# Performance work log

Measured on AMD Instinct MI355X. Metric: run time of the kernel, lower is better.

The kernel has to match this reference:

```python
import jax, jax.numpy as jnp
import numpy as np

N_NODES = 100000
N_EDGES = 1600000
F_IN = 128
UNITS = 128


def setup_inputs() -> dict:
    key = jax.random.key(0)
    k1, k2, k3, k4, k5 = jax.random.split(key, 5)
    X = jax.random.normal(k1, (N_NODES, F_IN), dtype=jnp.float32)
    edge_row = jnp.sort(jax.random.randint(k2, (N_EDGES,), 0, N_NODES, dtype=jnp.int64))
    edge_col = jax.random.randint(k3, (N_EDGES,), 0, N_NODES, dtype=jnp.int64)
    edge_val = jax.random.uniform(k4, (N_EDGES,), dtype=jnp.float32)
    weight = jax.random.normal(k5, (F_IN, UNITS), dtype=jnp.float32) * (1.0 / np.sqrt(F_IN))
    bias = jnp.zeros((UNITS,), dtype=jnp.float32)
    return {"X": X, "edge_row": edge_row, "edge_col": edge_col,
            "edge_val": edge_val, "weight": weight, "bias": bias}


def reference(X, edge_row, edge_col, edge_val, weight, bias):
    # h = X @ W  (dense feature transform)
    h = jnp.matmul(X, weight)                      # [N, units]
    # output = An @ h  as sparse SpMM: gather source rows, scale, scatter-add
    msg = edge_val[:, None] * h[edge_col]          # [E, units]
    agg = jax.ops.segment_sum(msg, edge_row, num_segments=N_NODES)  # [N, units]
    # bias add + sigmoid activation
    return jax.nn.sigmoid(agg + bias)
```

## Files before the change

### kernel.cpp

```cpp
#include <hip/hip_runtime.h>
#include <cstddef>

#define F 128
#define LDB 136

typedef __attribute__((ext_vector_type(8))) short bf16x8;
typedef __attribute__((ext_vector_type(4))) float f32x4;

__device__ __forceinline__ unsigned short f2bf(float f) {
  unsigned int u = __float_as_uint(f);
  u += 0x7fffu + ((u >> 16) & 1u);
  return (unsigned short)(u >> 16);
}

__global__ __launch_bounds__(256) void setup(const int* __restrict__ erow,
                                             int n_edges, int n_nodes, int nbA,
                                             int* __restrict__ row_ptr,
                                             const float* __restrict__ W,
                                             unsigned short* __restrict__ Wt) {
  const int bid = blockIdx.x;
  if (bid < nbA) {
    const int e = bid * 256 + threadIdx.x;
    if (e > n_edges) return;
    int r_lo, r_hi, val;
    if (e == 0) {
      r_lo = 0; r_hi = erow[0]; val = 0;
    } else if (e == n_edges) {
      r_lo = erow[n_edges - 1] + 1; r_hi = n_nodes; val = n_edges;
    } else {
      const int rp = erow[e - 1], rc = erow[e];
      r_lo = rp + 1; r_hi = rc; val = e;
    }
    for (int r = r_lo; r <= r_hi; ++r) row_ptr[r] = val;
  } else {
    const int idx = (bid - nbA) * 256 + threadIdx.x;
    const int k = idx >> 7, n = idx & 127;
    Wt[n * F + k] = f2bf(W[idx]);
  }
}

__global__ __launch_bounds__(256) void gemm_mfma(const float* __restrict__ X,
                                                 const unsigned short* __restrict__ Wt,
                                                 unsigned short* __restrict__ H,
                                                 int n_nodes) {
  __shared__ alignas(16) unsigned short Bs[128 * LDB];
  const int tid = threadIdx.x;

  {
    const uint4* src = (const uint4*)Wt;
    #pragma unroll
    for (int i = 0; i < 8; ++i) {
      const int idx = tid + i * 256;
      const int n = idx >> 4, c8 = idx & 15;
      *(uint4*)&Bs[n * LDB + c8 * 8] = src[idx];
    }
  }
  __syncthreads();

  const int wave = tid >> 6;
  const int lane = tid & 63;
  const int l15 = lane & 15;
  const int quad = lane >> 4;
  const int rbase = blockIdx.x * 128 + wave * 32;

  const float* xr[2];
  #pragma unroll
  for (int rt = 0; rt < 2; ++rt) {
    int r = rbase + rt * 16 + l15;
    if (r > n_nodes - 1) r = n_nodes - 1;
    xr[rt] = X + (size_t)r * F;
  }

  f32x4 acc[2][8] = {};

  #pragma unroll
  for (int ks = 0; ks < 4; ++ks) {
    const int k0 = ks * 32 + quad * 8;
    bf16x8 a[2], b[8];
    #pragma unroll
    for (int rt = 0; rt < 2; ++rt) {
      const float4 x0 = *(const float4*)(xr[rt] + k0);
      const float4 x1 = *(const float4*)(xr[rt] + k0 + 4);
      bf16x8 t;
      t[0] = (short)f2bf(x0.x); t[1] = (short)f2bf(x0.y);
      t[2] = (short)f2bf(x0.z); t[3] = (short)f2bf(x0.w);
      t[4] = (short)f2bf(x1.x); t[5] = (short)f2bf(x1.y);
      t[6] = (short)f2bf(x1.z); t[7] = (short)f2bf(x1.w);
      a[rt] = t;
    }
    #pragma unroll
    for (int ct = 0; ct < 8; ++ct)
      b[ct] = *(const bf16x8*)&Bs[(ct * 16 + l15) * LDB + k0];
    #pragma unroll
    for (int rt = 0; rt < 2; ++rt)
      #pragma unroll
      for (int ct = 0; ct < 8; ++ct)
        acc[rt][ct] = __builtin_amdgcn_mfma_f32_16x16x32_bf16(
            b[ct], a[rt], acc[rt][ct], 0, 0, 0);
  }

  #pragma unroll
  for (int rt = 0; rt < 2; ++rt) {
    const int row = rbase + rt * 16 + l15;
    if (row < n_nodes) {
      #pragma unroll
      for (int ct = 0; ct < 8; ++ct) {
        const unsigned int d0 = (unsigned int)f2bf(acc[rt][ct][0]) |
                                ((unsigned int)f2bf(acc[rt][ct][1]) << 16);
        const unsigned int d1 = (unsigned int)f2bf(acc[rt][ct][2]) |
                                ((unsigned int)f2bf(acc[rt][ct][3]) << 16);
        uint2 u; u.x = d0; u.y = d1;
        *(uint2*)&H[(size_t)row * F + ct * 16 + quad * 4] = u;
      }
    }
  }
}

__global__ __launch_bounds__(256) void spmm_bias_sigmoid(
    const int* __restrict__ row_ptr, const int* __restrict__ ecol,
    const float* __restrict__ eval, const unsigned short* __restrict__ H,
    const float* __restrict__ bias, float* __restrict__ out, int n_nodes) {
  const int wave = threadIdx.x >> 6;
  const int lane = threadIdx.x & 63;
  const int g = lane >> 4;
  const int fl = lane & 15;
  const int node = blockIdx.x * 16 + wave * 4 + g;
  const bool valid = (node < n_nodes);

  const int lo = valid ? row_ptr[node] : 0;
  const int hi = valid ? row_ptr[node + 1] : 0;
  const int deg = hi - lo;

  int dmax = deg;
  dmax = max(dmax, __shfl_xor(dmax, 16, 64));
  dmax = max(dmax, __shfl_xor(dmax, 32, 64));

  const int bpbase = (lane & 48) * 4;
  const char* Hb = (const char*)H + fl * 16;

  float acc[8] = {};

#define SPMM_STEP(j)                                                        \
  {                                                                         \
    const int idx = bpbase + (j) * 4;                                       \
    const int ro = __builtin_amdgcn_ds_bpermute(idx, voff);                 \
    const float v = __int_as_float(                                         \
        __builtin_amdgcn_ds_bpermute(idx, __float_as_int(vv)));             \
    const uint4 h = *(const uint4*)(Hb + ro);                               \
    acc[0] += v * __uint_as_float(h.x << 16);                               \
    acc[1] += v * __uint_as_float(h.x & 0xffff0000u);                       \
    acc[2] += v * __uint_as_float(h.y << 16);                               \
    acc[3] += v * __uint_as_float(h.y & 0xffff0000u);                       \
    acc[4] += v * __uint_as_float(h.z << 16);                               \
    acc[5] += v * __uint_as_float(h.z & 0xffff0000u);                       \
    acc[6] += v * __uint_as_float(h.w << 16);                               \
    acc[7] += v * __uint_as_float(h.w & 0xffff0000u);                       \
  }

  for (int base = 0; base < dmax; base += 16) {
    int voff = 0;
    float vv = 0.f;
    if (base + fl < deg) {
      const int e = lo + base + fl;
      voff = ecol[e] << 8;
      vv = eval[e];
    }
    const int cnt = min(dmax - base, 16);
    if (cnt == 16) {
      #pragma unroll
      for (int j = 0; j < 16; ++j) SPMM_STEP(j)
    } else {
      #pragma unroll 4
      for (int j = 0; j < cnt; ++j) SPMM_STEP(j)
    }
  }
#undef SPMM_STEP

  if (valid) {
    const float4 b0 = *(const float4*)&bias[fl * 8];
    const float4 b1 = *(const float4*)&bias[fl * 8 + 4];
    float4 o0, o1;
    o0.x = 1.f / (1.f + expf(-(acc[0] + b0.x)));
    o0.y = 1.f / (1.f + expf(-(acc[1] + b0.y)));
    o0.z = 1.f / (1.f + expf(-(acc[2] + b0.z)));
    o0.w = 1.f / (1.f + expf(-(acc[3] + b0.w)));
    o1.x = 1.f / (1.f + expf(-(acc[4] + b1.x)));
    o1.y = 1.f / (1.f + expf(-(acc[5] + b1.y)));
    o1.z = 1.f / (1.f + expf(-(acc[6] + b1.z)));
    o1.w = 1.f / (1.f + expf(-(acc[7] + b1.w)));
    float* op = out + (size_t)node * F + fl * 8;
    *(float4*)op = o0;
    *(float4*)(op + 4) = o1;
  }
}

extern "C" void kernel_launch(void* const* d_in, const int* in_sizes, int n_in,
                              void* d_out, int out_size, void* d_ws, size_t ws_size,
                              hipStream_t stream) {
  const float* X    = (const float*)d_in[0];
  const int*   erow = (const int*)  d_in[1];
  const int*   ecol = (const int*)  d_in[2];
  const float* eval = (const float*)d_in[3];
  const float* W    = (const float*)d_in[4];
  const float* bias = (const float*)d_in[5];
  float* out = (float*)d_out;

  const int n_nodes = in_sizes[0] / F;
  const int n_edges = in_sizes[1];

  char* ws = (char*)d_ws;
  unsigned short* H = (unsigned short*)ws;
  size_t off = (size_t)n_nodes * F * sizeof(unsigned short);
  int* row_ptr = (int*)(ws + off);
  off += ((size_t)(n_nodes + 1) * sizeof(int) + 15) & ~(size_t)15;
  unsigned short* Wt = (unsigned short*)(ws + off);

  const int nbA = (n_edges + 256) / 256;
  const int nbB = (F * F) / 256;
  setup<<<nbA + nbB, 256, 0, stream>>>(erow, n_edges, n_nodes, nbA, row_ptr,
                                       W, Wt);
  gemm_mfma<<<(n_nodes + 127) / 128, 256, 0, stream>>>(X, Wt, H, n_nodes);
  spmm_bias_sigmoid<<<(n_nodes + 15) / 16, 256, 0, stream>>>(
      row_ptr, ecol, eval, H, bias, out, n_nodes);
}
```

Baseline: 189.7 us.

## Slice H into 16-feature column panels and process SpMM per feature slice

The GEMM now writes H as eight column-major panels of 16 bf16 features each (32 bytes per node per panel). The SpMM kernel is split across 8 feature-slice blocks per 128-node tile. Each pair of lanes owns one node and walks its edges with 4-wide nontemporal loads of col/val, replacing the earlier 16-lane cooperative gather with ds_bpermute broadcasts. The intent is for each panel (about 3.2 MB) to fit in cache so gathers hit L2, at the cost of reading edge lists eight times and uneven per-lane degree work within a wave.

```diff
diff --git a/kernel.cpp b/kernel.cpp
--- a/kernel.cpp
+++ b/kernel.cpp
@@ -6,6 +6,7 @@
 
 typedef __attribute__((ext_vector_type(8))) short bf16x8;
 typedef __attribute__((ext_vector_type(4))) float f32x4;
+typedef __attribute__((ext_vector_type(4))) unsigned int u32x4;
 
 __device__ __forceinline__ unsigned short f2bf(float f) {
   unsigned int u = __float_as_uint(f);
@@ -99,6 +100,7 @@
             b[ct], a[rt], acc[rt][ct], 0, 0, 0);
   }
 
+  const size_t ns16 = (size_t)n_nodes * 16;
   #pragma unroll
   for (int rt = 0; rt < 2; ++rt) {
     const int row = rbase + rt * 16 + l15;
@@ -110,87 +112,74 @@
         const unsigned int d1 = (unsigned int)f2bf(acc[rt][ct][2]) |
                                 ((unsigned int)f2bf(acc[rt][ct][3]) << 16);
         uint2 u; u.x = d0; u.y = d1;
-        *(uint2*)&H[(size_t)row * F + ct * 16 + quad * 4] = u;
+        *(uint2*)&H[ns16 * ct + (size_t)row * 16 + quad * 4] = u;
       }
     }
   }
+}
+
+__device__ __forceinline__ void fma8(float* acc, uint4 h, float v) {
+  acc[0] += v * __uint_as_float(h.x << 16);
+  acc[1] += v * __uint_as_float(h.x & 0xffff0000u);
+  acc[2] += v * __uint_as_float(h.y << 16);
+  acc[3] += v * __uint_as_float(h.y & 0xffff0000u);
+  acc[4] += v * __uint_as_float(h.z << 16);
+  acc[5] += v * __uint_as_float(h.z & 0xffff0000u);
+  acc[6] += v * __uint_as_float(h.w << 16);
+  acc[7] += v * __uint_as_float(h.w & 0xffff0000u);
 }
 
 __global__ __launch_bounds__(256) void spmm_bias_sigmoid(
     const int* __restrict__ row_ptr, const int* __restrict__ ecol,
     const float* __restrict__ eval, const unsigned short* __restrict__ H,
     const float* __restrict__ bias, float* __restrict__ out, int n_nodes) {
+  const int fb = blockIdx.x & 7;
+  const int nb = blockIdx.x >> 3;
+  const int lane = threadIdx.x & 63;
   const int wave = threadIdx.x >> 6;
-  const int lane = threadIdx.x & 63;
-  const int g = lane >> 4;
-  const int fl = lane & 15;
-  const int node = blockIdx.x * 16 + wave * 4 + g;
+  const int p = lane & 1;
+  const int node = nb * 128 + wave * 32 + (lane >> 1);
   const bool valid = (node < n_nodes);
 
-  const int lo = valid ? row_ptr[node] : 0;
-  const int hi = valid ? row_ptr[node + 1] : 0;
-  const int deg = hi - lo;
-
-  int dmax = deg;
-  dmax = max(dmax, __shfl_xor(dmax, 16, 64));
-  dmax = max(dmax, __shfl_xor(dmax, 32, 64));
-
-  const int bpbase = (lane & 48) * 4;
-  const char* Hb = (const char*)H + fl * 16;
+  int lo = 0, deg = 0;
+  if (valid) {
+    lo = row_ptr[node];
+    deg = row_ptr[node + 1] - lo;
+  }
+
+  const char* Hs = (const char*)H + (size_t)fb * ((size_t)n_nodes * 32) +
+                   (size_t)(p * 16);
 
   float acc[8] = {};
 
-#define SPMM_STEP(j)                                                        \
-  {                                                                         \
-    const int idx = bpbase + (j) * 4;                                       \
-    const int ro = __builtin_amdgcn_ds_bpermute(idx, voff);                 \
-    const float v = __int_as_float(                                         \
-        __builtin_amdgcn_ds_bpermute(idx, __float_as_int(vv)));             \
-    const uint4 h = *(const uint4*)(Hb + ro);                               \
-    acc[0] += v * __uint_as_float(h.x << 16);                               \
-    acc[1] += v * __uint_as_float(h.x & 0xffff0000u);                       \
-    acc[2] += v * __uint_as_float(h.y << 16);                               \
-    acc[3] += v * __uint_as_float(h.y & 0xffff0000u);                       \
-    acc[4] += v * __uint_as_float(h.z << 16);                               \
-    acc[5] += v * __uint_as_float(h.z & 0xffff0000u);                       \
-    acc[6] += v * __uint_as_float(h.w << 16);                               \
-    acc[7] += v * __uint_as_float(h.w & 0xffff0000u);                       \
-  }
-
-  for (int base = 0; base < dmax; base += 16) {
-    int voff = 0;
-    float vv = 0.f;
-    if (base + fl < deg) {
-      const int e = lo + base + fl;
-      voff = ecol[e] << 8;
-      vv = eval[e];
-    }
-    const int cnt = min(dmax - base, 16);
-    if (cnt == 16) {
-      #pragma unroll
-      for (int j = 0; j < 16; ++j) SPMM_STEP(j)
-    } else {
-      #pragma unroll 4
-      for (int j = 0; j < cnt; ++j) SPMM_STEP(j)
-    }
-  }
-#undef SPMM_STEP
+  const int abase = lo & ~3;
+  const int aend = (lo + deg + 3) & ~3;
+  for (int e0 = abase; e0 < aend; e0 += 4) {
+    const u32x4 cols = __builtin_nontemporal_load((const u32x4*)(ecol + e0));
+    const f32x4 vals = __builtin_nontemporal_load((const f32x4*)(eval + e0));
+    #pragma unroll
+    for (int j = 0; j < 4; ++j) {
+      const unsigned rel = (unsigned)(e0 + j - lo);
+      const float v = (rel < (unsigned)deg) ? vals[j] : 0.f;
+      const uint4 h = *(const uint4*)(Hs + ((size_t)cols[j] << 5));
+      fma8(acc, h, v);
+    }
+  }
 
   if (valid) {
-    const float4 b0 = *(const float4*)&bias[fl * 8];
-    const float4 b1 = *(const float4*)&bias[fl * 8 + 4];
-    float4 o0, o1;
-    o0.x = 1.f / (1.f + expf(-(acc[0] + b0.x)));
-    o0.y = 1.f / (1.f + expf(-(acc[1] + b0.y)));
-    o0.z = 1.f / (1.f + expf(-(acc[2] + b0.z)));
-    o0.w = 1.f / (1.f + expf(-(acc[3] + b0.w)));
-    o1.x = 1.f / (1.f + expf(-(acc[4] + b1.x)));
-    o1.y = 1.f / (1.f + expf(-(acc[5] + b1.y)));
-    o1.z = 1.f / (1.f + expf(-(acc[6] + b1.z)));
-    o1.w = 1.f / (1.f + expf(-(acc[7] + b1.w)));
-    float* op = out + (size_t)node * F + fl * 8;
-    *(float4*)op = o0;
-    *(float4*)(op + 4) = o1;
+    const float* bp = bias + fb * 16 + p * 8;
+    f32x4 o0, o1;
+    o0[0] = 1.f / (1.f + expf(-(acc[0] + bp[0])));
+    o0[1] = 1.f / (1.f + expf(-(acc[1] + bp[1])));
+    o0[2] = 1.f / (1.f + expf(-(acc[2] + bp[2])));
+    o0[3] = 1.f / (1.f + expf(-(acc[3] + bp[3])));
+    o1[0] = 1.f / (1.f + expf(-(acc[4] + bp[4])));
+    o1[1] = 1.f / (1.f + expf(-(acc[5] + bp[5])));
+    o1[2] = 1.f / (1.f + expf(-(acc[6] + bp[6])));
+    o1[3] = 1.f / (1.f + expf(-(acc[7] + bp[7])));
+    float* op = out + (size_t)node * F + fb * 16 + p * 8;
+    __builtin_nontemporal_store(o0, (f32x4*)op);
+    __builtin_nontemporal_store(o1, (f32x4*)(op + 4));
   }
 }
 
@@ -220,6 +209,7 @@
   setup<<<nbA + nbB, 256, 0, stream>>>(erow, n_edges, n_nodes, nbA, row_ptr,
                                        W, Wt);
   gemm_mfma<<<(n_nodes + 127) / 128, 256, 0, stream>>>(X, Wt, H, n_nodes);
-  spmm_bias_sigmoid<<<(n_nodes + 15) / 16, 256, 0, stream>>>(
+  const int nbN = (n_nodes + 127) / 128;
+  spmm_bias_sigmoid<<<nbN * 8, 256, 0, stream>>>(
       row_ptr, ecol, eval, H, bias, out, n_nodes);
 }
```

Measured after the change: 298.7 us. +57.5%, slower.
